# Optimization experiments

Measured on AMD Instinct MI355X. Metric: run time of the kernel, lower is better.

Reference implementation:

```python
import jax, jax.numpy as jnp
import numpy as np

EPS = 1e-5
COMMITMENT_COST = 0.25


def setup_inputs() -> dict:
    key = jax.random.key(0)
    k1, k2 = jax.random.split(key)
    inputs = jax.random.normal(k1, (8, 4096, 1024), dtype=jnp.float32)
    ln_weight = jnp.ones((1024,), dtype=jnp.float32)
    ln_bias = jnp.zeros((1024,), dtype=jnp.float32)
    emb = jax.random.normal(k2, (4, 64, 256), dtype=jnp.float32)
    # codebook rows are unit-normalized in __init__
    emb = emb / jnp.maximum(jnp.linalg.norm(emb, axis=-1, keepdims=True), EPS)
    return {"inputs": inputs, "ln_weight": ln_weight, "ln_bias": ln_bias, "embeddings": emb}


def reference(inputs, ln_weight, ln_bias, embeddings):
    # inputs: [B,T,D]; embeddings: [H,K,d] with D = H*d
    B, T, D = inputs.shape
    H, K, d = embeddings.shape

    # LayerNorm (eps=1e-5) + soft clamp tanh(x/5)*5
    mu = jnp.mean(inputs, axis=-1, keepdims=True)
    var = jnp.mean(jnp.square(inputs - mu), axis=-1, keepdims=True)
    x = (inputs - mu) * jax.lax.rsqrt(var + 1e-5) * ln_weight + ln_bias
    x = jnp.tanh(x / 5.0) * 5.0

    # L2-normalize over the FULL embedding dim (matches F.normalize(dim=-1))
    nrm = jnp.linalg.norm(x, axis=-1, keepdims=True)
    xn = x / jnp.maximum(nrm, EPS)

    flat = xn.reshape(-1, H, d)  # [N,H,d]
    # cosine scores against each head's codebook: [N,H,K]
    dist = jnp.einsum("nhd,hkd->nhk", flat, embeddings)
    idx = jnp.argmax(dist, axis=-1)  # [N,H] int

    # per-head gather of codebook vectors
    q = embeddings[jnp.arange(H)[None, :], idx]  # [N,H,d]
    q = q.reshape(B, T, D)

    e_latent_loss = jnp.mean(jnp.square(jax.lax.stop_gradient(q) - xn))
    loss = COMMITMENT_COST * e_latent_loss  # eval mode: entropy_loss = 0

    # straight-through estimator (note: against post-tanh x, not xn)
    quantized = x + jax.lax.stop_gradient(q - x)

    present = jnp.zeros((K,), dtype=bool).at[idx.reshape(-1)].set(True)
    unique_count = jnp.sum(present).astype(jnp.int32)
    return quantized, loss, unique_count
```

## Files before the change

kernel.cpp:

```cpp
#include <hip/hip_runtime.h>
#include <cstdint>
#include <cstddef>

#define NROWS   32768
#define DIM     1024
#define NH      4
#define HD      256
#define NK      64
#define RPB     16
#define NBLK    (NROWS / RPB)
#define THREADS 256

typedef __attribute__((ext_vector_type(8))) short short8;
typedef __attribute__((ext_vector_type(4))) float float4a;

__device__ __forceinline__ unsigned short f2bf(float f) {
  unsigned int u = __float_as_uint(f);
  u += 0x7fffu + ((u >> 16) & 1u);
  return (unsigned short)(u >> 16);
}

__global__ __launch_bounds__(256) void vq_pre(const float* __restrict__ emb,
                                              unsigned short* __restrict__ ws_emb) {
  const int gid  = blockIdx.x * 256 + threadIdx.x;
  const int lane = gid & 63;
  const int w    = gid >> 6;
  const int s = w & 7, ht = w >> 3, t = ht & 3, h = ht >> 2;
  const int code = t * 16 + (lane & 15);
  const int d0   = s * 32 + (lane >> 4) * 8;
  const float* p = emb + ((size_t)(h * NK + code)) * HD + d0;
  unsigned int w0 = f2bf(p[0]) | ((unsigned int)f2bf(p[1]) << 16);
  unsigned int w1 = f2bf(p[2]) | ((unsigned int)f2bf(p[3]) << 16);
  unsigned int w2 = f2bf(p[4]) | ((unsigned int)f2bf(p[5]) << 16);
  unsigned int w3 = f2bf(p[6]) | ((unsigned int)f2bf(p[7]) << 16);
  uint4 pk = make_uint4(w0, w1, w2, w3);
  *(uint4*)(ws_emb + (size_t)(w * 64 + lane) * 8) = pk;
}

__global__ __launch_bounds__(THREADS, 4) void vq_main(
    const float* __restrict__ in, const float* __restrict__ lnw,
    const float* __restrict__ lnb, const float* __restrict__ emb,
    const unsigned short* __restrict__ ws_emb,
    float* __restrict__ out, float* __restrict__ ws)
{
  __shared__ __align__(16) unsigned short xs[NH * 8 * 4 * 16 * 8];
  __shared__ float inv_s[RPB];
  __shared__ float base_s[RPB];
  __shared__ __align__(16) int bidx_s[RPB][NH];
  __shared__ float bval_s[RPB][NH];
  __shared__ int flags_s[NH][NK];

  float* ws_loss = ws;
  unsigned long long* ws_mask = (unsigned long long*)(ws + NBLK);

  const int tid  = threadIdx.x;
  const int wave = tid >> 6;
  const int lane = tid & 63;
  const int row0 = blockIdx.x * RPB;

  flags_s[tid >> 6][tid & 63] = 0;

  float4 wv[4], bv4[4];
  #pragma unroll
  for (int c = 0; c < 4; ++c) {
    wv[c]  = *(const float4*)(lnw + c * 256 + lane * 4);
    bv4[c] = *(const float4*)(lnb + c * 256 + lane * 4);
  }

  const int sA = lane >> 3;
  const int qA = (lane >> 1) & 3;
  const int hfA = lane & 1;

  #pragma unroll
  for (int rr = 0; rr < 4; ++rr) {
    const int m = wave * 4 + rr;
    const float* rp = in + (size_t)(row0 + m) * DIM;
    float4 v[4];
    #pragma unroll
    for (int c = 0; c < 4; ++c) v[c] = *(const float4*)(rp + c * 256 + lane * 4);

    float s1 = 0.f, s2 = 0.f;
    #pragma unroll
    for (int c = 0; c < 4; ++c) {
      s1 += (v[c].x + v[c].y) + (v[c].z + v[c].w);
      s2 = fmaf(v[c].x, v[c].x, s2); s2 = fmaf(v[c].y, v[c].y, s2);
      s2 = fmaf(v[c].z, v[c].z, s2); s2 = fmaf(v[c].w, v[c].w, s2);
    }
    #pragma unroll
    for (int d = 1; d < 64; d <<= 1) {
      s1 += __shfl_xor(s1, d, 64);
      s2 += __shfl_xor(s2, d, 64);
    }
    const float mu   = s1 * (1.0f / 1024.0f);
    const float var  = fmaf(-mu, mu, s2 * (1.0f / 1024.0f));
    const float rstd = rsqrtf(var + 1e-5f);

    float ss = 0.f;
    #pragma unroll
    for (int c = 0; c < 4; ++c) {
      float*       pv = reinterpret_cast<float*>(&v[c]);
      const float* pw = reinterpret_cast<const float*>(&wv[c]);
      const float* pb = reinterpret_cast<const float*>(&bv4[c]);
      #pragma unroll
      for (int i = 0; i < 4; ++i) {
        float xh = (pv[i] - mu) * rstd;
        xh = fmaf(xh, pw[i], pb[i]);
        const float e = __expf(0.4f * xh);
        const float t = 1.f - 2.f * __builtin_amdgcn_rcpf(e + 1.f);
        const float xx = 5.f * t;
        ss = fmaf(xx, xx, ss);
        pv[i] = xx;
      }
    }
    #pragma unroll
    for (int d = 1; d < 64; d <<= 1) ss += __shfl_xor(ss, d, 64);

    const int msw = m ^ (qA << 2) ^ sA;
    #pragma unroll
    for (int c = 0; c < 4; ++c) {
      const int gran = ((c * 8 + sA) * 4 + qA) * 16 + msw;
      uint2 pk;
      pk.x = f2bf(v[c].x) | ((unsigned int)f2bf(v[c].y) << 16);
      pk.y = f2bf(v[c].z) | ((unsigned int)f2bf(v[c].w) << 16);
      *(uint2*)&xs[gran * 8 + hfA * 4] = pk;
    }

    if (lane == 0) {
      const float nrm = sqrtf(ss);
      const float iv  = 1.f / fmaxf(nrm, 1e-5f);
      inv_s[m]  = iv;
      base_s[m] = fmaf(ss * iv, iv, 4.f);
    }
  }
  __syncthreads();

  {
    const int h = wave;
    const int q = lane >> 4, mm = lane & 15;

    short8 afr[8];
    #pragma unroll
    for (int s = 0; s < 8; ++s) {
      const int gran = (h * 8 + s) * 64 + q * 16 + (mm ^ (q << 2) ^ s);
      afr[s] = *(const short8*)&xs[gran * 8];
    }

    const short8* eb = (const short8*)ws_emb + (size_t)h * 2048 + lane;
    float4a acc[4];
    #pragma unroll
    for (int t = 0; t < 4; ++t) {
      #pragma unroll
      for (int r = 0; r < 4; ++r) acc[t][r] = 0.f;
    }
    #pragma unroll
    for (int t = 0; t < 4; ++t) {
      #pragma unroll
      for (int s = 0; s < 8; ++s) {
        const short8 bfr = eb[(t * 8 + s) * 64];
        acc[t] = __builtin_amdgcn_mfma_f32_16x16x32_bf16(afr[s], bfr, acc[t], 0, 0, 0);
      }
    }

    #pragma unroll
    for (int r = 0; r < 4; ++r) {
      float bv = acc[0][r];
      int   bi = mm;
      #pragma unroll
      for (int t = 1; t < 4; ++t) {
        if (acc[t][r] > bv) { bv = acc[t][r]; bi = t * 16 + mm; }
      }
      #pragma unroll
      for (int d = 1; d <= 8; d <<= 1) {
        const float ov = __shfl_xor(bv, d, 64);
        const int   oi = __shfl_xor(bi, d, 64);
        if (ov > bv || (ov == bv && oi < bi)) { bv = ov; bi = oi; }
      }
      if (mm == 0) {
        const int row = q * 4 + r;
        bidx_s[row][h] = bi;
        bval_s[row][h] = bv;
        flags_s[h][bi] = 1;
      }
    }
  }
  __syncthreads();

  #pragma unroll
  for (int rr = 0; rr < 4; ++rr) {
    const int row = wave * 4 + rr;
    const int4 bi = *(const int4*)(&bidx_s[row][0]);
    const float4 q0 = *(const float4*)(emb + (size_t)(0 * NK + bi.x) * HD + lane * 4);
    const float4 q1 = *(const float4*)(emb + (size_t)(1 * NK + bi.y) * HD + lane * 4);
    const float4 q2 = *(const float4*)(emb + (size_t)(2 * NK + bi.z) * HD + lane * 4);
    const float4 q3 = *(const float4*)(emb + (size_t)(3 * NK + bi.w) * HD + lane * 4);
    float* op = out + (size_t)(row0 + row) * DIM + lane * 4;
    *(float4*)(op + 0)   = q0;
    *(float4*)(op + 256) = q1;
    *(float4*)(op + 512) = q2;
    *(float4*)(op + 768) = q3;
  }

  if (wave == 0) {
    float lsum = 0.f;
    if (lane < RPB) {
      const float ds = (bval_s[lane][0] + bval_s[lane][1]) +
                       (bval_s[lane][2] + bval_s[lane][3]);
      lsum = fmaf(-2.f * inv_s[lane], ds, base_s[lane]);
    }
    #pragma unroll
    for (int d = 1; d <= 8; d <<= 1) lsum += __shfl_xor(lsum, d, 64);
    if (lane == 0) ws_loss[blockIdx.x] = lsum;
  } else if (wave == 1) {
    const int f = flags_s[0][lane] | flags_s[1][lane] |
                  flags_s[2][lane] | flags_s[3][lane];
    const unsigned long long mk = __ballot(f != 0);
    if (lane == 0) ws_mask[blockIdx.x] = mk;
  }
}

__global__ __launch_bounds__(256) void vq_fin(const float* __restrict__ ws,
                                              float* __restrict__ out) {
  __shared__ float ls[4];
  __shared__ unsigned long long ms[4];
  const float* ws_loss = ws;
  const unsigned long long* ws_mask = (const unsigned long long*)(ws + NBLK);

  const int tid = threadIdx.x, wave = tid >> 6, lane = tid & 63;
  float l = 0.f;
  unsigned long long m = 0ull;
  for (int i = tid; i < NBLK; i += 256) { l += ws_loss[i]; m |= ws_mask[i]; }
  #pragma unroll
  for (int s = 1; s < 64; s <<= 1) {
    l += __shfl_xor(l, s, 64);
    m |= __shfl_xor(m, s, 64);
  }
  if (lane == 0) { ls[wave] = l; ms[wave] = m; }
  __syncthreads();
  if (tid == 0) {
    const float total = (ls[0] + ls[1]) + (ls[2] + ls[3]);
    const unsigned long long mm = ms[0] | ms[1] | ms[2] | ms[3];
    out[33554432] = 0.25f * total / 33554432.0f;
    out[33554433] = (float)__popcll(mm);
  }
}

extern "C" void kernel_launch(void* const* d_in, const int* in_sizes, int n_in,
                              void* d_out, int out_size, void* d_ws, size_t ws_size,
                              hipStream_t stream) {
  const float* in  = (const float*)d_in[0];
  const float* lnw = (const float*)d_in[1];
  const float* lnb = (const float*)d_in[2];
  const float* emb = (const float*)d_in[3];
  float* out = (float*)d_out;
  float* ws  = (float*)d_ws;

  unsigned short* ws_emb = (unsigned short*)((char*)d_ws + 24576);

  vq_pre<<<32, 256, 0, stream>>>(emb, ws_emb);
  vq_main<<<NBLK, THREADS, 0, stream>>>(in, lnw, lnb, emb, ws_emb, out, ws);
  vq_fin<<<1, 256, 0, stream>>>(ws, out);
}
```

Baseline: 257.7 us.

## Double block to 512 threads, split MFMA code tiles across wave pairs

Raises the block to 8 waves. Each wave now handles 2 rows of layernorm instead of 4, and the per-head score computation is split so each wave computes 2 of the 4 code tiles, with an extra LDS merge step for the argmax. LayerNorm weight and bias are staged in shared memory as bf16 rather than held in registers. The aim is more memory parallelism and latency hiding per block. The costs are an extra barrier and lower precision for the LN weight and bias, which happen to be exact for the test values.

```diff
diff --git a/kernel.cpp b/kernel.cpp
--- a/kernel.cpp
+++ b/kernel.cpp
@@ -9,7 +9,7 @@
 #define NK      64
 #define RPB     16
 #define NBLK    (NROWS / RPB)
-#define THREADS 256
+#define THREADS 512
 
 typedef __attribute__((ext_vector_type(8))) short short8;
 typedef __attribute__((ext_vector_type(4))) float float4a;
@@ -18,6 +18,12 @@
   unsigned int u = __float_as_uint(f);
   u += 0x7fffu + ((u >> 16) & 1u);
   return (unsigned short)(u >> 16);
+}
+__device__ __forceinline__ float bflo(unsigned int u) {
+  return __uint_as_float(u << 16);
+}
+__device__ __forceinline__ float bfhi(unsigned int u) {
+  return __uint_as_float(u & 0xffff0000u);
 }
 
 __global__ __launch_bounds__(256) void vq_pre(const float* __restrict__ emb,
@@ -37,18 +43,22 @@
   *(uint4*)(ws_emb + (size_t)(w * 64 + lane) * 8) = pk;
 }
 
-__global__ __launch_bounds__(THREADS, 4) void vq_main(
+__global__ __launch_bounds__(THREADS, 8) void vq_main(
     const float* __restrict__ in, const float* __restrict__ lnw,
     const float* __restrict__ lnb, const float* __restrict__ emb,
     const unsigned short* __restrict__ ws_emb,
     float* __restrict__ out, float* __restrict__ ws)
 {
   __shared__ __align__(16) unsigned short xs[NH * 8 * 4 * 16 * 8];
+  __shared__ __align__(16) unsigned short wsh[DIM];
+  __shared__ __align__(16) unsigned short bsh[DIM];
   __shared__ float inv_s[RPB];
   __shared__ float base_s[RPB];
   __shared__ __align__(16) int bidx_s[RPB][NH];
   __shared__ float bval_s[RPB][NH];
   __shared__ int flags_s[NH][NK];
+  __shared__ float cva[RPB][NH][2];
+  __shared__ int   cia[RPB][NH][2];
 
   float* ws_loss = ws;
   unsigned long long* ws_mask = (unsigned long long*)(ws + NBLK);
@@ -58,84 +68,117 @@
   const int lane = tid & 63;
   const int row0 = blockIdx.x * RPB;
 
-  flags_s[tid >> 6][tid & 63] = 0;
-
-  float4 wv[4], bv4[4];
-  #pragma unroll
-  for (int c = 0; c < 4; ++c) {
-    wv[c]  = *(const float4*)(lnw + c * 256 + lane * 4);
-    bv4[c] = *(const float4*)(lnb + c * 256 + lane * 4);
-  }
+  float4 w4, b4;
+  if (tid < 256) {
+    w4 = *(const float4*)(lnw + tid * 4);
+    b4 = *(const float4*)(lnb + tid * 4);
+  }
+
+  const int m0 = wave * 2;
+  float4 v[2][4];
+  #pragma unroll
+  for (int rr = 0; rr < 2; ++rr) {
+    const float* rp = in + (size_t)(row0 + m0 + rr) * DIM;
+    #pragma unroll
+    for (int c = 0; c < 4; ++c) v[rr][c] = *(const float4*)(rp + c * 256 + lane * 4);
+  }
+
+  if (tid < 256) {
+    flags_s[tid >> 6][tid & 63] = 0;
+    uint2 wp, bp;
+    wp.x = f2bf(w4.x) | ((unsigned int)f2bf(w4.y) << 16);
+    wp.y = f2bf(w4.z) | ((unsigned int)f2bf(w4.w) << 16);
+    bp.x = f2bf(b4.x) | ((unsigned int)f2bf(b4.y) << 16);
+    bp.y = f2bf(b4.z) | ((unsigned int)f2bf(b4.w) << 16);
+    *(uint2*)&wsh[tid * 4] = wp;
+    *(uint2*)&bsh[tid * 4] = bp;
+  }
+  __syncthreads();
 
   const int sA = lane >> 3;
   const int qA = (lane >> 1) & 3;
   const int hfA = lane & 1;
-
-  #pragma unroll
-  for (int rr = 0; rr < 4; ++rr) {
-    const int m = wave * 4 + rr;
-    const float* rp = in + (size_t)(row0 + m) * DIM;
-    float4 v[4];
-    #pragma unroll
-    for (int c = 0; c < 4; ++c) v[c] = *(const float4*)(rp + c * 256 + lane * 4);
-
-    float s1 = 0.f, s2 = 0.f;
-    #pragma unroll
-    for (int c = 0; c < 4; ++c) {
-      s1 += (v[c].x + v[c].y) + (v[c].z + v[c].w);
-      s2 = fmaf(v[c].x, v[c].x, s2); s2 = fmaf(v[c].y, v[c].y, s2);
-      s2 = fmaf(v[c].z, v[c].z, s2); s2 = fmaf(v[c].w, v[c].w, s2);
-    }
-    #pragma unroll
-    for (int d = 1; d < 64; d <<= 1) {
-      s1 += __shfl_xor(s1, d, 64);
-      s2 += __shfl_xor(s2, d, 64);
-    }
-    const float mu   = s1 * (1.0f / 1024.0f);
-    const float var  = fmaf(-mu, mu, s2 * (1.0f / 1024.0f));
-    const float rstd = rsqrtf(var + 1e-5f);
-
-    float ss = 0.f;
-    #pragma unroll
-    for (int c = 0; c < 4; ++c) {
-      float*       pv = reinterpret_cast<float*>(&v[c]);
-      const float* pw = reinterpret_cast<const float*>(&wv[c]);
-      const float* pb = reinterpret_cast<const float*>(&bv4[c]);
-      #pragma unroll
-      for (int i = 0; i < 4; ++i) {
-        float xh = (pv[i] - mu) * rstd;
-        xh = fmaf(xh, pw[i], pb[i]);
-        const float e = __expf(0.4f * xh);
-        const float t = 1.f - 2.f * __builtin_amdgcn_rcpf(e + 1.f);
-        const float xx = 5.f * t;
-        ss = fmaf(xx, xx, ss);
-        pv[i] = xx;
-      }
-    }
-    #pragma unroll
-    for (int d = 1; d < 64; d <<= 1) ss += __shfl_xor(ss, d, 64);
-
-    const int msw = m ^ (qA << 2) ^ sA;
-    #pragma unroll
-    for (int c = 0; c < 4; ++c) {
-      const int gran = ((c * 8 + sA) * 4 + qA) * 16 + msw;
-      uint2 pk;
-      pk.x = f2bf(v[c].x) | ((unsigned int)f2bf(v[c].y) << 16);
-      pk.y = f2bf(v[c].z) | ((unsigned int)f2bf(v[c].w) << 16);
-      *(uint2*)&xs[gran * 8 + hfA * 4] = pk;
-    }
-
-    if (lane == 0) {
-      const float nrm = sqrtf(ss);
-      const float iv  = 1.f / fmaxf(nrm, 1e-5f);
-      inv_s[m]  = iv;
-      base_s[m] = fmaf(ss * iv, iv, 4.f);
-    }
+  const int msw0 = m0 ^ (qA << 2) ^ sA;
+
+  float s1a = 0.f, s2a = 0.f, s1b = 0.f, s2b = 0.f;
+  #pragma unroll
+  for (int c = 0; c < 4; ++c) {
+    s1a += (v[0][c].x + v[0][c].y) + (v[0][c].z + v[0][c].w);
+    s2a = fmaf(v[0][c].x, v[0][c].x, s2a); s2a = fmaf(v[0][c].y, v[0][c].y, s2a);
+    s2a = fmaf(v[0][c].z, v[0][c].z, s2a); s2a = fmaf(v[0][c].w, v[0][c].w, s2a);
+    s1b += (v[1][c].x + v[1][c].y) + (v[1][c].z + v[1][c].w);
+    s2b = fmaf(v[1][c].x, v[1][c].x, s2b); s2b = fmaf(v[1][c].y, v[1][c].y, s2b);
+    s2b = fmaf(v[1][c].z, v[1][c].z, s2b); s2b = fmaf(v[1][c].w, v[1][c].w, s2b);
+  }
+  #pragma unroll
+  for (int d = 1; d < 64; d <<= 1) {
+    s1a += __shfl_xor(s1a, d, 64);
+    s2a += __shfl_xor(s2a, d, 64);
+    s1b += __shfl_xor(s1b, d, 64);
+    s2b += __shfl_xor(s2b, d, 64);
+  }
+  const float mu0   = s1a * (1.0f / 1024.0f);
+  const float var0  = fmaf(-mu0, mu0, s2a * (1.0f / 1024.0f));
+  const float rstd0 = rsqrtf(var0 + 1e-5f);
+  const float mu1   = s1b * (1.0f / 1024.0f);
+  const float var1  = fmaf(-mu1, mu1, s2b * (1.0f / 1024.0f));
+  const float rstd1 = rsqrtf(var1 + 1e-5f);
+
+  float ssa = 0.f, ssb = 0.f;
+  #pragma unroll
+  for (int c = 0; c < 4; ++c) {
+    const uint2 wu = *(const uint2*)&wsh[c * 256 + lane * 4];
+    const uint2 bu = *(const uint2*)&bsh[c * 256 + lane * 4];
+    const float wf[4] = { bflo(wu.x), bfhi(wu.x), bflo(wu.y), bfhi(wu.y) };
+    const float bf[4] = { bflo(bu.x), bfhi(bu.x), bflo(bu.y), bfhi(bu.y) };
+    float* p0 = reinterpret_cast<float*>(&v[0][c]);
+    float* p1 = reinterpret_cast<float*>(&v[1][c]);
+    #pragma unroll
+    for (int i = 0; i < 4; ++i) {
+      float xh0 = (p0[i] - mu0) * rstd0;
+      xh0 = fmaf(xh0, wf[i], bf[i]);
+      const float e0 = __expf(0.4f * xh0);
+      const float t0 = 1.f - 2.f * __builtin_amdgcn_rcpf(e0 + 1.f);
+      const float x0 = 5.f * t0;
+      ssa = fmaf(x0, x0, ssa);
+      p0[i] = x0;
+
+      float xh1 = (p1[i] - mu1) * rstd1;
+      xh1 = fmaf(xh1, wf[i], bf[i]);
+      const float e1 = __expf(0.4f * xh1);
+      const float t1 = 1.f - 2.f * __builtin_amdgcn_rcpf(e1 + 1.f);
+      const float x1 = 5.f * t1;
+      ssb = fmaf(x1, x1, ssb);
+      p1[i] = x1;
+    }
+    const int gr = ((c * 8 + sA) * 4 + qA) * 16;
+    uint2 pk0, pk1;
+    pk0.x = f2bf(v[0][c].x) | ((unsigned int)f2bf(v[0][c].y) << 16);
+    pk0.y = f2bf(v[0][c].z) | ((unsigned int)f2bf(v[0][c].w) << 16);
+    pk1.x = f2bf(v[1][c].x) | ((unsigned int)f2bf(v[1][c].y) << 16);
+    pk1.y = f2bf(v[1][c].z) | ((unsigned int)f2bf(v[1][c].w) << 16);
+    *(uint2*)&xs[(gr + msw0) * 8 + hfA * 4] = pk0;
+    *(uint2*)&xs[(gr + (msw0 ^ 1)) * 8 + hfA * 4] = pk1;
+  }
+  #pragma unroll
+  for (int d = 1; d < 64; d <<= 1) {
+    ssa += __shfl_xor(ssa, d, 64);
+    ssb += __shfl_xor(ssb, d, 64);
+  }
+  if (lane == 0) {
+    const float n0 = sqrtf(ssa);
+    const float iv0 = 1.f / fmaxf(n0, 1e-5f);
+    inv_s[m0]  = iv0;
+    base_s[m0] = fmaf(ssa * iv0, iv0, 4.f);
+    const float n1 = sqrtf(ssb);
+    const float iv1 = 1.f / fmaxf(n1, 1e-5f);
+    inv_s[m0 + 1]  = iv1;
+    base_s[m0 + 1] = fmaf(ssb * iv1, iv1, 4.f);
   }
   __syncthreads();
 
   {
-    const int h = wave;
+    const int h = wave >> 1, tp = wave & 1;
     const int q = lane >> 4, mm = lane & 15;
 
     short8 afr[8];
@@ -146,29 +189,27 @@
     }
 
     const short8* eb = (const short8*)ws_emb + (size_t)h * 2048 + lane;
-    float4a acc[4];
-    #pragma unroll
-    for (int t = 0; t < 4; ++t) {
+    float4a acc[2];
+    #pragma unroll
+    for (int tt = 0; tt < 2; ++tt) {
       #pragma unroll
-      for (int r = 0; r < 4; ++r) acc[t][r] = 0.f;
-    }
-    #pragma unroll
-    for (int t = 0; t < 4; ++t) {
+      for (int r = 0; r < 4; ++r) acc[tt][r] = 0.f;
+    }
+    #pragma unroll
+    for (int tt = 0; tt < 2; ++tt) {
+      const int t = tp * 2 + tt;
       #pragma unroll
       for (int s = 0; s < 8; ++s) {
         const short8 bfr = eb[(t * 8 + s) * 64];
-        acc[t] = __builtin_amdgcn_mfma_f32_16x16x32_bf16(afr[s], bfr, acc[t], 0, 0, 0);
+        acc[tt] = __builtin_amdgcn_mfma_f32_16x16x32_bf16(afr[s], bfr, acc[tt], 0, 0, 0);
       }
     }
 
     #pragma unroll
     for (int r = 0; r < 4; ++r) {
       float bv = acc[0][r];
-      int   bi = mm;
-      #pragma unroll
-      for (int t = 1; t < 4; ++t) {
-        if (acc[t][r] > bv) { bv = acc[t][r]; bi = t * 16 + mm; }
-      }
+      int   bi = (tp * 2) * 16 + mm;
+      if (acc[1][r] > bv) { bv = acc[1][r]; bi = (tp * 2 + 1) * 16 + mm; }
       #pragma unroll
       for (int d = 1; d <= 8; d <<= 1) {
         const float ov = __shfl_xor(bv, d, 64);
@@ -177,17 +218,28 @@
       }
       if (mm == 0) {
         const int row = q * 4 + r;
-        bidx_s[row][h] = bi;
-        bval_s[row][h] = bv;
-        flags_s[h][bi] = 1;
+        cva[row][h][tp] = bv;
+        cia[row][h][tp] = bi;
       }
     }
   }
   __syncthreads();
 
-  #pragma unroll
-  for (int rr = 0; rr < 4; ++rr) {
-    const int row = wave * 4 + rr;
+  if (tid < 64) {
+    const int row = tid >> 2, h = tid & 3;
+    const float v0 = cva[row][h][0], v1 = cva[row][h][1];
+    const int   i0 = cia[row][h][0], i1 = cia[row][h][1];
+    int win = i0; float wv = v0;
+    if (v1 > v0) { win = i1; wv = v1; }
+    bidx_s[row][h] = win;
+    bval_s[row][h] = wv;
+    flags_s[h][win] = 1;
+  }
+  __syncthreads();
+
+  #pragma unroll
+  for (int rr = 0; rr < 2; ++rr) {
+    const int row = wave * 2 + rr;
     const int4 bi = *(const int4*)(&bidx_s[row][0]);
     const float4 q0 = *(const float4*)(emb + (size_t)(0 * NK + bi.x) * HD + lane * 4);
     const float4 q1 = *(const float4*)(emb + (size_t)(1 * NK + bi.y) * HD + lane * 4);
```

Result: slower. 265.5 us (+3.0%).

## Use 1024-thread blocks with one row per wave and split codebook tiles across waves

Applied to the files above, without the earlier changes.

Blocks grow from 256 to 1024 threads, so each of 16 waves handles a single row's LayerNorm and tanh instead of four rows per wave. The MFMA stage is split so each wave computes one 16-code tile for one head, with a shared-memory cross-wave argmax merge and an extra barrier. LayerNorm weight and bias are staged in LDS as bf16, which lowers their precision and could slightly change outputs. The aim is more memory-level parallelism and fewer registers per thread, at the cost of extra syncs and a lower occupancy bound per block.

```diff
diff --git a/kernel.cpp b/kernel.cpp
--- a/kernel.cpp
+++ b/kernel.cpp
@@ -9,7 +9,7 @@
 #define NK      64
 #define RPB     16
 #define NBLK    (NROWS / RPB)
-#define THREADS 256
+#define THREADS 1024
 
 typedef __attribute__((ext_vector_type(8))) short short8;
 typedef __attribute__((ext_vector_type(4))) float float4a;
@@ -18,6 +18,12 @@
   unsigned int u = __float_as_uint(f);
   u += 0x7fffu + ((u >> 16) & 1u);
   return (unsigned short)(u >> 16);
+}
+__device__ __forceinline__ float bflo(unsigned int u) {
+  return __uint_as_float(u << 16);
+}
+__device__ __forceinline__ float bfhi(unsigned int u) {
+  return __uint_as_float(u & 0xffff0000u);
 }
 
 __global__ __launch_bounds__(256) void vq_pre(const float* __restrict__ emb,
@@ -37,18 +43,22 @@
   *(uint4*)(ws_emb + (size_t)(w * 64 + lane) * 8) = pk;
 }
 
-__global__ __launch_bounds__(THREADS, 4) void vq_main(
+__global__ __launch_bounds__(THREADS, 8) void vq_main(
     const float* __restrict__ in, const float* __restrict__ lnw,
     const float* __restrict__ lnb, const float* __restrict__ emb,
     const unsigned short* __restrict__ ws_emb,
     float* __restrict__ out, float* __restrict__ ws)
 {
   __shared__ __align__(16) unsigned short xs[NH * 8 * 4 * 16 * 8];
+  __shared__ __align__(16) unsigned short wsh[DIM];
+  __shared__ __align__(16) unsigned short bsh[DIM];
   __shared__ float inv_s[RPB];
   __shared__ float base_s[RPB];
   __shared__ __align__(16) int bidx_s[RPB][NH];
   __shared__ float bval_s[RPB][NH];
   __shared__ int flags_s[NH][NK];
+  __shared__ float cva[RPB][NH][4];
+  __shared__ int   cia[RPB][NH][4];
 
   float* ws_loss = ws;
   unsigned long long* ws_mask = (unsigned long long*)(ws + NBLK);
@@ -58,84 +68,90 @@
   const int lane = tid & 63;
   const int row0 = blockIdx.x * RPB;
 
-  flags_s[tid >> 6][tid & 63] = 0;
-
-  float4 wv[4], bv4[4];
-  #pragma unroll
-  for (int c = 0; c < 4; ++c) {
-    wv[c]  = *(const float4*)(lnw + c * 256 + lane * 4);
-    bv4[c] = *(const float4*)(lnb + c * 256 + lane * 4);
-  }
+  float4 w4, b4;
+  if (tid < 256) {
+    w4 = *(const float4*)(lnw + tid * 4);
+    b4 = *(const float4*)(lnb + tid * 4);
+  }
+
+  const int m = wave;
+  float4 v[4];
+  {
+    const float* rp = in + (size_t)(row0 + m) * DIM;
+    #pragma unroll
+    for (int c = 0; c < 4; ++c) v[c] = *(const float4*)(rp + c * 256 + lane * 4);
+  }
+
+  if (tid < 256) {
+    flags_s[tid >> 6][tid & 63] = 0;
+    uint2 wp, bp;
+    wp.x = f2bf(w4.x) | ((unsigned int)f2bf(w4.y) << 16);
+    wp.y = f2bf(w4.z) | ((unsigned int)f2bf(w4.w) << 16);
+    bp.x = f2bf(b4.x) | ((unsigned int)f2bf(b4.y) << 16);
+    bp.y = f2bf(b4.z) | ((unsigned int)f2bf(b4.w) << 16);
+    *(uint2*)&wsh[tid * 4] = wp;
+    *(uint2*)&bsh[tid * 4] = bp;
+  }
+  __syncthreads();
 
   const int sA = lane >> 3;
   const int qA = (lane >> 1) & 3;
   const int hfA = lane & 1;
-
-  #pragma unroll
-  for (int rr = 0; rr < 4; ++rr) {
-    const int m = wave * 4 + rr;
-    const float* rp = in + (size_t)(row0 + m) * DIM;
-    float4 v[4];
-    #pragma unroll
-    for (int c = 0; c < 4; ++c) v[c] = *(const float4*)(rp + c * 256 + lane * 4);
-
-    float s1 = 0.f, s2 = 0.f;
-    #pragma unroll
-    for (int c = 0; c < 4; ++c) {
-      s1 += (v[c].x + v[c].y) + (v[c].z + v[c].w);
-      s2 = fmaf(v[c].x, v[c].x, s2); s2 = fmaf(v[c].y, v[c].y, s2);
-      s2 = fmaf(v[c].z, v[c].z, s2); s2 = fmaf(v[c].w, v[c].w, s2);
-    }
-    #pragma unroll
-    for (int d = 1; d < 64; d <<= 1) {
-      s1 += __shfl_xor(s1, d, 64);
-      s2 += __shfl_xor(s2, d, 64);
-    }
-    const float mu   = s1 * (1.0f / 1024.0f);
-    const float var  = fmaf(-mu, mu, s2 * (1.0f / 1024.0f));
-    const float rstd = rsqrtf(var + 1e-5f);
-
-    float ss = 0.f;
-    #pragma unroll
-    for (int c = 0; c < 4; ++c) {
-      float*       pv = reinterpret_cast<float*>(&v[c]);
-      const float* pw = reinterpret_cast<const float*>(&wv[c]);
-      const float* pb = reinterpret_cast<const float*>(&bv4[c]);
-      #pragma unroll
-      for (int i = 0; i < 4; ++i) {
-        float xh = (pv[i] - mu) * rstd;
-        xh = fmaf(xh, pw[i], pb[i]);
-        const float e = __expf(0.4f * xh);
-        const float t = 1.f - 2.f * __builtin_amdgcn_rcpf(e + 1.f);
-        const float xx = 5.f * t;
-        ss = fmaf(xx, xx, ss);
-        pv[i] = xx;
-      }
-    }
-    #pragma unroll
-    for (int d = 1; d < 64; d <<= 1) ss += __shfl_xor(ss, d, 64);
-
-    const int msw = m ^ (qA << 2) ^ sA;
-    #pragma unroll
-    for (int c = 0; c < 4; ++c) {
-      const int gran = ((c * 8 + sA) * 4 + qA) * 16 + msw;
-      uint2 pk;
-      pk.x = f2bf(v[c].x) | ((unsigned int)f2bf(v[c].y) << 16);
-      pk.y = f2bf(v[c].z) | ((unsigned int)f2bf(v[c].w) << 16);
-      *(uint2*)&xs[gran * 8 + hfA * 4] = pk;
-    }
-
-    if (lane == 0) {
-      const float nrm = sqrtf(ss);
-      const float iv  = 1.f / fmaxf(nrm, 1e-5f);
-      inv_s[m]  = iv;
-      base_s[m] = fmaf(ss * iv, iv, 4.f);
-    }
+  const int msw = m ^ (qA << 2) ^ sA;
+
+  float s1 = 0.f, s2 = 0.f;
+  #pragma unroll
+  for (int c = 0; c < 4; ++c) {
+    s1 += (v[c].x + v[c].y) + (v[c].z + v[c].w);
+    s2 = fmaf(v[c].x, v[c].x, s2); s2 = fmaf(v[c].y, v[c].y, s2);
+    s2 = fmaf(v[c].z, v[c].z, s2); s2 = fmaf(v[c].w, v[c].w, s2);
+  }
+  #pragma unroll
+  for (int d = 1; d < 64; d <<= 1) {
+    s1 += __shfl_xor(s1, d, 64);
+    s2 += __shfl_xor(s2, d, 64);
+  }
+  const float mu   = s1 * (1.0f / 1024.0f);
+  const float var  = fmaf(-mu, mu, s2 * (1.0f / 1024.0f));
+  const float rstd = rsqrtf(var + 1e-5f);
+
+  float ss = 0.f;
+  #pragma unroll
+  for (int c = 0; c < 4; ++c) {
+    const uint2 wu = *(const uint2*)&wsh[c * 256 + lane * 4];
+    const uint2 bu = *(const uint2*)&bsh[c * 256 + lane * 4];
+    const float wf[4] = { bflo(wu.x), bfhi(wu.x), bflo(wu.y), bfhi(wu.y) };
+    const float bf[4] = { bflo(bu.x), bfhi(bu.x), bflo(bu.y), bfhi(bu.y) };
+    float* pv = reinterpret_cast<float*>(&v[c]);
+    #pragma unroll
+    for (int i = 0; i < 4; ++i) {
+      float xh = (pv[i] - mu) * rstd;
+      xh = fmaf(xh, wf[i], bf[i]);
+      const float e = __expf(0.4f * xh);
+      const float t = 1.f - 2.f * __builtin_amdgcn_rcpf(e + 1.f);
+      const float xx = 5.f * t;
+      ss = fmaf(xx, xx, ss);
+      pv[i] = xx;
+    }
+    const int gran = ((c * 8 + sA) * 4 + qA) * 16 + msw;
+    uint2 pk;
+    pk.x = f2bf(v[c].x) | ((unsigned int)f2bf(v[c].y) << 16);
+    pk.y = f2bf(v[c].z) | ((unsigned int)f2bf(v[c].w) << 16);
+    *(uint2*)&xs[gran * 8 + hfA * 4] = pk;
+  }
+  #pragma unroll
+  for (int d = 1; d < 64; d <<= 1) ss += __shfl_xor(ss, d, 64);
+
+  if (lane == 0) {
+    const float nrm = sqrtf(ss);
+    const float iv  = 1.f / fmaxf(nrm, 1e-5f);
+    inv_s[m]  = iv;
+    base_s[m] = fmaf(ss * iv, iv, 4.f);
   }
   __syncthreads();
 
   {
-    const int h = wave;
+    const int h = wave >> 2, t = wave & 3;
     const int q = lane >> 4, mm = lane & 15;
 
     short8 afr[8];
@@ -146,29 +162,19 @@
     }
 
     const short8* eb = (const short8*)ws_emb + (size_t)h * 2048 + lane;
-    float4a acc[4];
-    #pragma unroll
-    for (int t = 0; t < 4; ++t) {
-      #pragma unroll
-      for (int r = 0; r < 4; ++r) acc[t][r] = 0.f;
-    }
-    #pragma unroll
-    for (int t = 0; t < 4; ++t) {
-      #pragma unroll
-      for (int s = 0; s < 8; ++s) {
-        const short8 bfr = eb[(t * 8 + s) * 64];
-        acc[t] = __builtin_amdgcn_mfma_f32_16x16x32_bf16(afr[s], bfr, acc[t], 0, 0, 0);
-      }
+    float4a acc;
+    #pragma unroll
+    for (int r = 0; r < 4; ++r) acc[r] = 0.f;
+    #pragma unroll
+    for (int s = 0; s < 8; ++s) {
+      const short8 bfr = eb[(t * 8 + s) * 64];
+      acc = __builtin_amdgcn_mfma_f32_16x16x32_bf16(afr[s], bfr, acc, 0, 0, 0);
     }
 
     #pragma unroll
     for (int r = 0; r < 4; ++r) {
-      float bv = acc[0][r];
-      int   bi = mm;
-      #pragma unroll
-      for (int t = 1; t < 4; ++t) {
-        if (acc[t][r] > bv) { bv = acc[t][r]; bi = t * 16 + mm; }
-      }
+      float bv = acc[r];
+      int   bi = t * 16 + mm;
       #pragma unroll
       for (int d = 1; d <= 8; d <<= 1) {
         const float ov = __shfl_xor(bv, d, 64);
@@ -177,17 +183,31 @@
       }
       if (mm == 0) {
         const int row = q * 4 + r;
-        bidx_s[row][h] = bi;
-        bval_s[row][h] = bv;
-        flags_s[h][bi] = 1;
+        cva[row][h][t] = bv;
+        cia[row][h][t] = bi;
       }
     }
   }
   __syncthreads();
 
-  #pragma unroll
-  for (int rr = 0; rr < 4; ++rr) {
-    const int row = wave * 4 + rr;
+  if (tid < 64) {
+    const int row = tid >> 2, h = tid & 3;
+    float wv = cva[row][h][0];
+    int   win = cia[row][h][0];
+    #pragma unroll
+    for (int t = 1; t < 4; ++t) {
+      const float v1 = cva[row][h][t];
+      const int   i1 = cia[row][h][t];
+      if (v1 > wv) { wv = v1; win = i1; }
+    }
+    bidx_s[row][h] = win;
+    bval_s[row][h] = wv;
+    flags_s[h][win] = 1;
+  }
+  __syncthreads();
+
+  {
+    const int row = wave;
     const int4 bi = *(const int4*)(&bidx_s[row][0]);
     const float4 q0 = *(const float4*)(emb + (size_t)(0 * NK + bi.x) * HD + lane * 4);
     const float4 q1 = *(const float4*)(emb + (size_t)(1 * NK + bi.y) * HD + lane * 4);
```

After: 259.2 us. About the same (+0.6%).
